# Performance work log

Hardware: AMD Instinct MI355X
Metric: run time of the kernel (lower is better)

The kernel has to match this reference:

```python
import jax, jax.numpy as jnp
import numpy as np

B, N, C0, L = 4, 16, 64, 2048
C1 = C2 = C3 = 128
E = 16384
EPS = 1e-5


def setup_inputs() -> dict:
    key = jax.random.key(0)
    ks = jax.random.split(key, 8)
    x = jax.random.normal(ks[0], (B, N, C0, L), jnp.float32)
    edge_index = jax.random.randint(ks[1], (2, E), 0, L, dtype=jnp.int64)

    def xavier(k, fi, fo):
        s = (2.0 / (fi + fo)) ** 0.5
        return jax.random.normal(k, (fi, fo), jnp.float32) * s

    return dict(
        x=x, edge_index=edge_index,
        W1=xavier(ks[2], C0, C1), b1=jnp.zeros(C1), g1=jnp.ones(C1), be1=jnp.zeros(C1),
        W2=xavier(ks[3], C1, C2), b2=jnp.zeros(C2), g2=jnp.ones(C2), be2=jnp.zeros(C2),
        W3=xavier(ks[4], C2, C3), b3=jnp.zeros(C3), g3=jnp.ones(C3), be3=jnp.zeros(C3),
    )


def _gcn(h, src, dst, norm, self_coef, W, bias):
    # h: [G, L, Cin] -> [G, L, Cout]; improved GCN: A_hat = A + 2I, sym-normalized
    hw = h @ W
    msgs = hw[:, src] * norm[None, :, None]          # [G, E, Cout]
    agg = jnp.zeros_like(hw).at[:, dst].add(msgs)     # scatter-add to targets
    return agg + self_coef[None, :, None] * hw + bias


def _center_bn_relu(h, g, be):
    # h: [G, L, C] -> [G, C, L]; mean-center over set dim n, BatchNorm1d (train), ReLU
    G, Lx, C = h.shape
    z = h.transpose(0, 2, 1).reshape(B, N, C, Lx)
    z = z - z.mean(axis=1, keepdims=True)
    z = z.reshape(G, C, Lx)
    mu = z.mean(axis=(0, 2), keepdims=True)
    var = z.var(axis=(0, 2), keepdims=True)           # biased, matches BN training
    z = (z - mu) / jnp.sqrt(var + EPS) * g[None, :, None] + be[None, :, None]
    return jnp.maximum(z, 0.0)


def reference(x, edge_index, W1, b1, g1, be1, W2, b2, g2, be2, W3, b3, g3, be3):
    b, n, c, l = x.shape
    src, dst = edge_index[0], edge_index[1]
    # improved=True: self-loop weight 2
    deg = jnp.zeros((l,), jnp.float32).at[dst].add(1.0) + 2.0
    dinv = 1.0 / jnp.sqrt(deg)
    norm = dinv[src] * dinv[dst]                      # per-edge coefficient
    self_coef = 2.0 * dinv * dinv                     # per-node self-loop coefficient

    h = x.reshape(b * n, c, l).transpose(0, 2, 1)     # [G, L, C0]

    h = _gcn(h, src, dst, norm, self_coef, W1, b1)
    z = _center_bn_relu(h, g1, be1)                   # [G, C1, L]
    h = z.transpose(0, 2, 1)

    h = _gcn(h, src, dst, norm, self_coef, W2, b2)
    z = _center_bn_relu(h, g2, be2)
    h = z.transpose(0, 2, 1)

    h = _gcn(h, src, dst, norm, self_coef, W3, b3)
    z = _center_bn_relu(h, g3, be3)                   # [G, C3, L]
    return z
```

## Files before the change

kernel.cpp:

```cpp
#include <hip/hip_runtime.h>
#include <hip/hip_bf16.h>

#define GG 64
#define LN 2048
#define BB 4
#define NS 16
#define EE 16384
#define C_0 64
#define CH 128
#define EPSV 1e-5f
#define VK 16
#define GNB 8
#define ECAP 384
#define SLICE ((size_t)LN * 1024)

using bf16x8 = __attribute__((ext_vector_type(8))) short;
using f32x4  = __attribute__((ext_vector_type(4))) float;
using u32x4  = __attribute__((ext_vector_type(4))) unsigned int;
typedef unsigned long long ull;

__device__ __forceinline__ float b2f(unsigned short u) {
    union { unsigned int i; float f; } v; v.i = ((unsigned int)u) << 16; return v.f;
}
__device__ __forceinline__ unsigned short f2b(float f) {
    union { float f; unsigned int i; } v; v.f = f;
    unsigned int r = v.i + 0x7fffu + ((v.i >> 16) & 1u);
    return (unsigned short)(r >> 16);
}
__device__ __forceinline__ void acc8(float* acc, u32x4 v, float w) {
    acc[0] += w * b2f((unsigned short)(v.x & 0xffffu));
    acc[1] += w * b2f((unsigned short)(v.x >> 16));
    acc[2] += w * b2f((unsigned short)(v.y & 0xffffu));
    acc[3] += w * b2f((unsigned short)(v.y >> 16));
    acc[4] += w * b2f((unsigned short)(v.z & 0xffffu));
    acc[5] += w * b2f((unsigned short)(v.z >> 16));
    acc[6] += w * b2f((unsigned short)(v.w & 0xffffu));
    acc[7] += w * b2f((unsigned short)(v.w >> 16));
}

__global__ void k_deg(const int* __restrict__ dst, int* __restrict__ cnt) {
    int e = blockIdx.x * blockDim.x + threadIdx.x;
    if (e < EE) atomicAdd(&cnt[dst[e]], 1);
}

__global__ void k_node(const int* __restrict__ cnt, float* __restrict__ dinv,
                       float* __restrict__ selfc) {
    int l = blockIdx.x * blockDim.x + threadIdx.x;
    if (l < LN) {
        float d = (float)cnt[l] + 2.0f;
        float di = rsqrtf(d);
        dinv[l] = di;
        selfc[l] = 2.0f * di * di;
    }
}

__global__ void k_scan(const int* __restrict__ cnt, int* __restrict__ off) {
    __shared__ int part[256];
    __shared__ int pre[256];
    int t = threadIdx.x;
    int base = t * 8;
    int loc[8];
    int s = 0;
#pragma unroll
    for (int i = 0; i < 8; i++) { loc[i] = cnt[base + i]; s += loc[i]; }
    part[t] = s;
    __syncthreads();
    if (t == 0) {
        int run = 0;
        for (int i = 0; i < 256; i++) { pre[i] = run; run += part[i]; }
        off[LN] = run;
    }
    __syncthreads();
    int run = pre[t];
#pragma unroll
    for (int i = 0; i < 8; i++) { off[base + i] = run; run += loc[i]; }
}

__global__ void k_fill(const int* __restrict__ src, const int* __restrict__ dst,
                       const int* __restrict__ off, int* __restrict__ cur,
                       const float* __restrict__ dinv, ull* __restrict__ epack) {
    int e = blockIdx.x * blockDim.x + threadIdx.x;
    if (e < EE) {
        int s = src[e], d = dst[e];
        int pos = atomicAdd(&cur[d], 1);
        int idx = off[d] + pos;
        union { float f; unsigned u; } w;
        w.f = dinv[s] * dinv[d];
        epack[idx] = (ull)(unsigned)s | ((ull)w.u << 32);
    }
}

__global__ void k_wprep(const float* __restrict__ W, unsigned short* __restrict__ Wp,
                        int K) {
    int idx = blockIdx.x * 256 + threadIdx.x;
    if (idx < K * CH) {
        int k = idx >> 7, c = idx & (CH - 1);
        int nf = c >> 4, lr = c & 15, ks = k >> 5, hi = (k >> 3) & 3, j = k & 7;
        Wp[(ks * 8 + nf) * 512 + (hi * 16 + lr) * 8 + j] = f2b(W[idx]);
    }
}

template <int K, bool FUSE>
__global__ __launch_bounds__(256) void k_mm(
    const float* __restrict__ X, const unsigned short* __restrict__ Ap,
    const float* __restrict__ scl, const float* __restrict__ bet,
    const unsigned short* __restrict__ Wp, unsigned short* __restrict__ hw)
{
    constexpr int KP = K + 8;
    __shared__ unsigned short As[64 * 136];
    const int g = blockIdx.y;
    const int l0 = blockIdx.x * 64;
    const int t = threadIdx.x;
    const int wq = t >> 6;
    const int lane = t & 63;
    const int lr = lane & 15;
    const int hi = lane >> 4;
    const int kof = hi * 8;

    f32x4 acc[8];
#pragma unroll
    for (int i = 0; i < 8; i++) acc[i] = (f32x4){0.f, 0.f, 0.f, 0.f};

    if (FUSE) {
        const int sg = g >> 5;
        const int gi = g & 31;
        const int row = l0 + wq * 16 + lr;
        bf16x8 aF[K / 32];
#pragma unroll
        for (int ks = 0; ks < K / 32; ks++) {
            const unsigned short* ap = Ap + (size_t)(sg * 4 + ks) * SLICE +
                                       (size_t)row * 1024 + gi * 32 + kof;
            union { uint4 v; unsigned short s[8]; } u;
            u.v = *(const uint4*)ap;
            const int cb = ks * 32 + kof;
            float4 s0 = *(const float4*)&scl[cb];
            float4 s1 = *(const float4*)&scl[cb + 4];
            float4 c0 = *(const float4*)&bet[cb];
            float4 c1 = *(const float4*)&bet[cb + 4];
            union { bf16x8 f; unsigned short s[8]; } o;
            o.s[0] = f2b(fmaxf(b2f(u.s[0]) * s0.x + c0.x, 0.f));
            o.s[1] = f2b(fmaxf(b2f(u.s[1]) * s0.y + c0.y, 0.f));
            o.s[2] = f2b(fmaxf(b2f(u.s[2]) * s0.z + c0.z, 0.f));
            o.s[3] = f2b(fmaxf(b2f(u.s[3]) * s0.w + c0.w, 0.f));
            o.s[4] = f2b(fmaxf(b2f(u.s[4]) * s1.x + c1.x, 0.f));
            o.s[5] = f2b(fmaxf(b2f(u.s[5]) * s1.y + c1.y, 0.f));
            o.s[6] = f2b(fmaxf(b2f(u.s[6]) * s1.z + c1.z, 0.f));
            o.s[7] = f2b(fmaxf(b2f(u.s[7]) * s1.w + c1.w, 0.f));
            aF[ks] = o.f;
        }
#pragma unroll
        for (int ks = 0; ks < K / 32; ks++) {
#pragma unroll
            for (int nf = 0; nf < 8; nf++) {
                bf16x8 bF = *(const bf16x8*)&Wp[(ks * 8 + nf) * 512 + lane * 8];
                acc[nf] = __builtin_amdgcn_mfma_f32_16x16x32_bf16(aF[ks], bF,
                                                                  acc[nf], 0, 0, 0);
            }
        }
    } else {
        const int k = t >> 2;
        const int lq = (t & 3) * 16;
        const float* xp = X + ((size_t)g * K + k) * LN + l0 + lq;
#pragma unroll
        for (int i = 0; i < 16; i += 4) {
            float4 v = *(const float4*)&xp[i];
            As[(lq + i + 0) * KP + k] = f2b(v.x);
            As[(lq + i + 1) * KP + k] = f2b(v.y);
            As[(lq + i + 2) * KP + k] = f2b(v.z);
            As[(lq + i + 3) * KP + k] = f2b(v.w);
        }
        __syncthreads();
#pragma unroll
        for (int ks = 0; ks < K / 32; ks++) {
            bf16x8 aF = *(const bf16x8*)&As[(wq * 16 + lr) * KP + ks * 32 + kof];
#pragma unroll
            for (int nf = 0; nf < 8; nf++) {
                bf16x8 bF = *(const bf16x8*)&Wp[(ks * 8 + nf) * 512 + lane * 8];
                acc[nf] = __builtin_amdgcn_mfma_f32_16x16x32_bf16(aF, bF,
                                                                  acc[nf], 0, 0, 0);
            }
        }
        __syncthreads();
    }
#pragma unroll
    for (int nf = 0; nf < 8; nf++) {
#pragma unroll
        for (int r = 0; r < 4; r++) {
            int row = wq * 16 + (lane >> 4) * 4 + r;
            int col = nf * 16 + lr;
            As[row * 136 + col] = f2b(acc[nf][r]);
        }
    }
    __syncthreads();
    {
        const int l = t >> 2;
        const int sc = t & 3;
        unsigned short* hp = hw + (size_t)((g >> 5) * 4 + sc) * SLICE +
                             (size_t)(l0 + l) * 1024 + (g & 31) * 32;
#pragma unroll
        for (int i = 0; i < 32; i += 8)
            *(uint4*)&hp[i] = *(const uint4*)&As[l * 136 + sc * 32 + i];
    }
}

__global__ __launch_bounds__(256) void k_gnv(
    const unsigned short* __restrict__ hw, unsigned short* __restrict__ a,
    float* __restrict__ varK, const int* __restrict__ off,
    const ull* __restrict__ epack, const float* __restrict__ selfc)
{
    __shared__ ull emeta[ECAP];
    __shared__ int soff[GNB + 1];
    __shared__ float sselfc[GNB];
    __shared__ float vred[4][32];
    const int bid = blockIdx.x;
    const int sid = bid & 7;
    const int chunk = bid >> 3;
    const int l0 = chunk * GNB;
    const int t = threadIdx.x;
    const int tr = t >> 7;
    const int ti = t & 127;
    const int lane = t & 63;
    const int wq = t >> 6;
    const int go = ti * 8;
    const unsigned short* hws = hw + sid * SLICE;
    unsigned short* aBs = a + sid * SLICE;

    u32x4 v0s[GNB / 2];
#pragma unroll
    for (int ii = 0; ii < GNB / 2; ii++)
        v0s[ii] = *(const u32x4*)&hws[(size_t)(l0 + ii * 2 + tr) * 1024 + go];

    const int e0 = off[l0];
    const int eTot = off[l0 + GNB] - e0;
    if (t <= GNB) soff[t] = off[l0 + t];
    if (t >= 32 && t < 32 + GNB) sselfc[t - 32] = selfc[l0 + t - 32];
    const int estg = eTot < ECAP ? eTot : ECAP;
    for (int i = t; i < estg; i += 256) emeta[i] = epack[e0 + i];
    __syncthreads();

    float vacc[8] = {0.f, 0.f, 0.f, 0.f, 0.f, 0.f, 0.f, 0.f};

    auto gather = [&](const ull* __restrict__ mp) {
#pragma unroll
        for (int ii = 0; ii < GNB / 2; ii++) {
            const int ln = ii * 2 + tr;
            const int l = l0 + ln;
            const int s0 = soff[ln] - e0;
            const int s1 = soff[ln + 1] - e0;
            const float sc = sselfc[ln];
            float acc[8];
            {
                u32x4 v0 = v0s[ii];
                acc[0] = sc * b2f((unsigned short)(v0.x & 0xffffu));
                acc[1] = sc * b2f((unsigned short)(v0.x >> 16));
                acc[2] = sc * b2f((unsigned short)(v0.y & 0xffffu));
                acc[3] = sc * b2f((unsigned short)(v0.y >> 16));
                acc[4] = sc * b2f((unsigned short)(v0.z & 0xffffu));
                acc[5] = sc * b2f((unsigned short)(v0.z >> 16));
                acc[6] = sc * b2f((unsigned short)(v0.w & 0xffffu));
                acc[7] = sc * b2f((unsigned short)(v0.w >> 16));
            }
            int e = s0;
            for (; e + 4 <= s1; e += 4) {
                ull m0 = mp[e], m1 = mp[e + 1], m2 = mp[e + 2], m3 = mp[e + 3];
                u32x4 vA = *(const u32x4*)&hws[(size_t)(unsigned)m0 * 1024 + go];
                u32x4 vB = *(const u32x4*)&hws[(size_t)(unsigned)m1 * 1024 + go];
                u32x4 vC = *(const u32x4*)&hws[(size_t)(unsigned)m2 * 1024 + go];
                u32x4 vD = *(const u32x4*)&hws[(size_t)(unsigned)m3 * 1024 + go];
                acc8(acc, vA, __uint_as_float((unsigned)(m0 >> 32)));
                acc8(acc, vB, __uint_as_float((unsigned)(m1 >> 32)));
                acc8(acc, vC, __uint_as_float((unsigned)(m2 >> 32)));
                acc8(acc, vD, __uint_as_float((unsigned)(m3 >> 32)));
            }
            for (; e < s1; e++) {
                ull m0 = mp[e];
                u32x4 vA = *(const u32x4*)&hws[(size_t)(unsigned)m0 * 1024 + go];
                acc8(acc, vA, __uint_as_float((unsigned)(m0 >> 32)));
            }
            float m[8];
#pragma unroll
            for (int j = 0; j < 8; j++) m[j] = acc[j];
#pragma unroll
            for (int mask = 4; mask <= 32; mask <<= 1) {
#pragma unroll
                for (int j = 0; j < 8; j++) m[j] += __shfl_xor(m[j], mask);
            }
            u32x4 o;
            unsigned short ob[8];
#pragma unroll
            for (int j = 0; j < 8; j++) {
                float d = acc[j] - m[j] * (1.f / NS);
                vacc[j] += d * d;
                ob[j] = f2b(d);
            }
            o.x = (unsigned int)ob[0] | ((unsigned int)ob[1] << 16);
            o.y = (unsigned int)ob[2] | ((unsigned int)ob[3] << 16);
            o.z = (unsigned int)ob[4] | ((unsigned int)ob[5] << 16);
            o.w = (unsigned int)ob[6] | ((unsigned int)ob[7] << 16);
            __builtin_nontemporal_store(o, (u32x4*)&aBs[(size_t)l * 1024 + go]);
        }
    };
    if (eTot <= ECAP) gather(emeta);
    else gather(epack + e0);

#pragma unroll
    for (int mask = 4; mask <= 32; mask <<= 1) {
#pragma unroll
        for (int j = 0; j < 8; j++) vacc[j] += __shfl_xor(vacc[j], mask);
    }
    if (lane < 4) {
#pragma unroll
        for (int j = 0; j < 8; j++) vred[wq][lane * 8 + j] = vacc[j];
    }
    __syncthreads();
    if (t < 32) {
        float s = vred[0][t] + vred[1][t] + vred[2][t] + vred[3][t];
        atomicAdd(&varK[(chunk & (VK - 1)) * CH + (sid & 3) * 32 + t], s);
    }
}

__global__ void k_scale(const float* __restrict__ varK, const float* __restrict__ gam,
                        float* __restrict__ scl) {
    int c = threadIdx.x;
    float v = 0.f;
#pragma unroll
    for (int k = 0; k < VK; k++) v += varK[k * CH + c];
    scl[c] = gam[c] * rsqrtf(v * (1.f / (GG * LN)) + EPSV);
}

__global__ __launch_bounds__(256) void k_epi_t(
    const unsigned short* __restrict__ a, const float* __restrict__ scl,
    const float* __restrict__ bet, float* __restrict__ out)
{
    __shared__ unsigned short lds[16 * 32 * 40];
    const int bid = blockIdx.x;
    const int sid = bid & 7;
    const int chunk = bid >> 3;
    const int l0 = chunk * 16;
    const int t = threadIdx.x;
    const int sg = sid >> 2;
    const int sc = sid & 3;
    const unsigned short* aBs = a + sid * SLICE;
    {
        const int tr = t >> 7;
        const int ti = t & 127;
        const int gl = ti >> 2;
        const int c0 = (ti & 3) * 8;
#pragma unroll
        for (int i = 0; i < 8; i++) {
            const int lloc = i * 2 + tr;
            uint4 v = *(const uint4*)&aBs[(size_t)(l0 + lloc) * 1024 + ti * 8];
            *(uint4*)&lds[(lloc * 32 + gl) * 40 + c0] = v;
        }
    }
    __syncthreads();
#pragma unroll
    for (int it = 0; it < 4; it++) {
        const int p = it * 256 + t;
        const int gl2 = p >> 5;
        const int c2 = p & 31;
        const int cG = sc * 32 + c2;
        const float s = scl[cG], bb = bet[cG];
        float o[16];
#pragma unroll
        for (int l = 0; l < 16; l++)
            o[l] = fmaxf(b2f(lds[(l * 32 + gl2) * 40 + c2]) * s + bb, 0.f);
        float* op = &out[((size_t)(sg * 32 + gl2) * CH + cG) * LN + l0];
#pragma unroll
        for (int l = 0; l < 16; l += 4)
            *(float4*)&op[l] = make_float4(o[l], o[l + 1], o[l + 2], o[l + 3]);
    }
}

extern "C" void kernel_launch(void* const* d_in, const int* in_sizes, int n_in,
                              void* d_out, int out_size, void* d_ws, size_t ws_size,
                              hipStream_t stream) {
    const float* x   = (const float*)d_in[0];
    const int*   ei  = (const int*)d_in[1];
    const float* W1  = (const float*)d_in[2];
    const float* g1  = (const float*)d_in[4];
    const float* be1 = (const float*)d_in[5];
    const float* W2  = (const float*)d_in[6];
    const float* g2  = (const float*)d_in[8];
    const float* be2 = (const float*)d_in[9];
    const float* W3  = (const float*)d_in[10];
    const float* g3  = (const float*)d_in[12];
    const float* be3 = (const float*)d_in[13];
    const int* srcp = ei;
    const int* dstp = ei + EE;

    char* ws = (char*)d_ws;
    size_t pos = 0;
    auto alloc = [&](size_t bytes) -> void* {
        void* p = ws + pos;
        pos = (pos + bytes + 255) & ~(size_t)255;
        return p;
    };
    const size_t big = (size_t)LN * GG * CH * sizeof(unsigned short);
    unsigned short* aB  = (unsigned short*)alloc(big);
    unsigned short* Wt1 = (unsigned short*)alloc(C_0 * CH * 2);
    unsigned short* Wt2 = (unsigned short*)alloc(CH * CH * 2);
    unsigned short* Wt3 = (unsigned short*)alloc(CH * CH * 2);
    int*   cnt   = (int*)alloc(LN * 4);
    int*   offA  = (int*)alloc((LN + 1) * 4);
    int*   cur   = (int*)alloc(LN * 4);
    float* dinv  = (float*)alloc(LN * 4);
    float* selfc = (float*)alloc(LN * 4);
    ull*   epack = (ull*)alloc(EE * 8);
    float* varK  = (float*)alloc(VK * CH * 4);
    float* scl   = (float*)alloc(CH * 4);
    unsigned short* hw = (ws_size >= pos + big) ? (unsigned short*)alloc(big)
                                                : (unsigned short*)d_out;

    hipMemsetAsync(cnt, 0, LN * 4, stream);
    hipMemsetAsync(cur, 0, LN * 4, stream);
    k_deg<<<EE / 256, 256, 0, stream>>>(dstp, cnt);
    k_node<<<LN / 256, 256, 0, stream>>>(cnt, dinv, selfc);
    k_scan<<<1, 256, 0, stream>>>(cnt, offA);
    k_fill<<<EE / 256, 256, 0, stream>>>(srcp, dstp, offA, cur, dinv, epack);
    k_wprep<<<(C_0 * CH) / 256, 256, 0, stream>>>(W1, Wt1, C_0);
    k_wprep<<<(CH * CH) / 256, 256, 0, stream>>>(W2, Wt2, CH);
    k_wprep<<<(CH * CH) / 256, 256, 0, stream>>>(W3, Wt3, CH);

    dim3 mmG(LN / 64, GG);
    const int gnvG = (LN / GNB) * 8;

    k_mm<C_0, false><<<mmG, 256, 0, stream>>>(x, nullptr, nullptr, nullptr, Wt1, hw);
    hipMemsetAsync(varK, 0, VK * CH * 4, stream);
    k_gnv<<<gnvG, 256, 0, stream>>>(hw, aB, varK, offA, epack, selfc);
    k_scale<<<1, CH, 0, stream>>>(varK, g1, scl);

    k_mm<CH, true><<<mmG, 256, 0, stream>>>(nullptr, aB, scl, be1, Wt2, hw);
    hipMemsetAsync(varK, 0, VK * CH * 4, stream);
    k_gnv<<<gnvG, 256, 0, stream>>>(hw, aB, varK, offA, epack, selfc);
    k_scale<<<1, CH, 0, stream>>>(varK, g2, scl);

    k_mm<CH, true><<<mmG, 256, 0, stream>>>(nullptr, aB, scl, be2, Wt3, hw);
    hipMemsetAsync(varK, 0, VK * CH * 4, stream);
    k_gnv<<<gnvG, 256, 0, stream>>>(hw, aB, varK, offA, epack, selfc);
    k_scale<<<1, CH, 0, stream>>>(varK, g3, scl);

    k_epi_t<<<128 * 8, 256, 0, stream>>>(aB, scl, be3, (float*)d_out);
}
```

Measured before the change: 244.2 us.

## Merge graph/weight prep into one kernel and fold BN scale into consumers

Replaces the degree, scan, fill and three weight-prep kernels plus two memsets with a single 7-block prep kernel. Graph CSR building now runs in one block using LDS atomics. The separate scale kernels and per-layer varK memsets are removed; each fused matmul and the epilogue recomputes the BN scale from the variance partials in LDS. The epilogue is also re-tiled to 32 rows by 16 groups per block. This cuts the launch count by about ten, at the cost of a serial single-block CSR build and redundant scale computation in every block.

```diff
diff --git a/kernel.cpp b/kernel.cpp
--- a/kernel.cpp
+++ b/kernel.cpp
@@ -37,77 +37,95 @@
     acc[6] += w * b2f((unsigned short)(v.w & 0xffffu));
     acc[7] += w * b2f((unsigned short)(v.w >> 16));
 }
-
-__global__ void k_deg(const int* __restrict__ dst, int* __restrict__ cnt) {
-    int e = blockIdx.x * blockDim.x + threadIdx.x;
-    if (e < EE) atomicAdd(&cnt[dst[e]], 1);
-}
-
-__global__ void k_node(const int* __restrict__ cnt, float* __restrict__ dinv,
-                       float* __restrict__ selfc) {
-    int l = blockIdx.x * blockDim.x + threadIdx.x;
-    if (l < LN) {
-        float d = (float)cnt[l] + 2.0f;
-        float di = rsqrtf(d);
-        dinv[l] = di;
-        selfc[l] = 2.0f * di * di;
-    }
-}
-
-__global__ void k_scan(const int* __restrict__ cnt, int* __restrict__ off) {
-    __shared__ int part[256];
-    __shared__ int pre[256];
-    int t = threadIdx.x;
-    int base = t * 8;
-    int loc[8];
-    int s = 0;
-#pragma unroll
-    for (int i = 0; i < 8; i++) { loc[i] = cnt[base + i]; s += loc[i]; }
-    part[t] = s;
-    __syncthreads();
-    if (t == 0) {
-        int run = 0;
-        for (int i = 0; i < 256; i++) { pre[i] = run; run += part[i]; }
-        off[LN] = run;
-    }
-    __syncthreads();
-    int run = pre[t];
-#pragma unroll
-    for (int i = 0; i < 8; i++) { off[base + i] = run; run += loc[i]; }
-}
-
-__global__ void k_fill(const int* __restrict__ src, const int* __restrict__ dst,
-                       const int* __restrict__ off, int* __restrict__ cur,
-                       const float* __restrict__ dinv, ull* __restrict__ epack) {
-    int e = blockIdx.x * blockDim.x + threadIdx.x;
-    if (e < EE) {
-        int s = src[e], d = dst[e];
-        int pos = atomicAdd(&cur[d], 1);
-        int idx = off[d] + pos;
-        union { float f; unsigned u; } w;
-        w.f = dinv[s] * dinv[d];
-        epack[idx] = (ull)(unsigned)s | ((ull)w.u << 32);
-    }
-}
-
-__global__ void k_wprep(const float* __restrict__ W, unsigned short* __restrict__ Wp,
-                        int K) {
-    int idx = blockIdx.x * 256 + threadIdx.x;
-    if (idx < K * CH) {
-        int k = idx >> 7, c = idx & (CH - 1);
-        int nf = c >> 4, lr = c & 15, ks = k >> 5, hi = (k >> 3) & 3, j = k & 7;
-        Wp[(ks * 8 + nf) * 512 + (hi * 16 + lr) * 8 + j] = f2b(W[idx]);
+__device__ __forceinline__ void wprep_one(const float* __restrict__ W,
+                                          unsigned short* __restrict__ Wp, int idx) {
+    int k = idx >> 7, c = idx & (CH - 1);
+    int nf = c >> 4, lr = c & 15, ks = k >> 5, hi = (k >> 3) & 3, j = k & 7;
+    Wp[(ks * 8 + nf) * 512 + (hi * 16 + lr) * 8 + j] = f2b(W[idx]);
+}
+
+__global__ __launch_bounds__(256) void k_prep(
+    const int* __restrict__ src, const int* __restrict__ dst,
+    const float* __restrict__ W1, const float* __restrict__ W2,
+    const float* __restrict__ W3,
+    float* __restrict__ selfc, int* __restrict__ off, ull* __restrict__ epack,
+    unsigned short* __restrict__ Wp1, unsigned short* __restrict__ Wp2,
+    unsigned short* __restrict__ Wp3, float* __restrict__ varK3)
+{
+    const int bid = blockIdx.x;
+    const int t = threadIdx.x;
+    if (bid == 0) {
+        __shared__ int cntL[LN];
+        __shared__ float dinvL[LN];
+        __shared__ int offL[LN + 1];
+        __shared__ int part[256];
+        __shared__ int pre2[256];
+        for (int i = t; i < LN; i += 256) cntL[i] = 0;
+        __syncthreads();
+        for (int e = t; e < EE; e += 256) atomicAdd(&cntL[dst[e]], 1);
+        __syncthreads();
+        for (int i = t; i < LN; i += 256) {
+            float d = (float)cntL[i] + 2.0f;
+            float di = rsqrtf(d);
+            dinvL[i] = di;
+            selfc[i] = 2.0f * di * di;
+        }
+        {
+            const int base = t * 8;
+            int loc[8];
+            int s = 0;
+#pragma unroll
+            for (int i = 0; i < 8; i++) { loc[i] = cntL[base + i]; s += loc[i]; }
+            part[t] = s;
+            __syncthreads();
+            if (t == 0) {
+                int run = 0;
+                for (int i = 0; i < 256; i++) { pre2[i] = run; run += part[i]; }
+                offL[LN] = run;
+                off[LN] = run;
+            }
+            __syncthreads();
+            int run = pre2[t];
+#pragma unroll
+            for (int i = 0; i < 8; i++) {
+                offL[base + i] = run;
+                off[base + i] = run;
+                run += loc[i];
+            }
+        }
+        __syncthreads();
+        for (int i = t; i < LN; i += 256) cntL[i] = 0;
+        __syncthreads();
+        for (int e = t; e < EE; e += 256) {
+            int s = src[e], d = dst[e];
+            int pos = atomicAdd(&cntL[d], 1);
+            union { float f; unsigned u; } w;
+            w.f = dinvL[s] * dinvL[d];
+            epack[offL[d] + pos] = (ull)(unsigned)s | ((ull)w.u << 32);
+        }
+    } else if (bid == 1) {
+        for (int i = t; i < C_0 * CH; i += 256) wprep_one(W1, Wp1, i);
+    } else if (bid <= 3) {
+        const int base = (bid - 2) * 8192;
+        for (int i = t; i < 8192; i += 256) wprep_one(W2, Wp2, base + i);
+    } else if (bid <= 5) {
+        const int base = (bid - 4) * 8192;
+        for (int i = t; i < 8192; i += 256) wprep_one(W3, Wp3, base + i);
+    } else {
+        for (int i = t; i < 3 * VK * CH; i += 256) varK3[i] = 0.f;
     }
 }
 
 template <int K, bool FUSE>
 __global__ __launch_bounds__(256) void k_mm(
     const float* __restrict__ X, const unsigned short* __restrict__ Ap,
-    const float* __restrict__ scl, const float* __restrict__ bet,
+    const float* __restrict__ varKp, const float* __restrict__ gam,
+    const float* __restrict__ bet,
     const unsigned short* __restrict__ Wp, unsigned short* __restrict__ hw)
 {
     constexpr int KP = K + 8;
     __shared__ unsigned short As[64 * 136];
+    __shared__ float sclL[CH];
     const int g = blockIdx.y;
     const int l0 = blockIdx.x * 64;
     const int t = threadIdx.x;
@@ -122,6 +140,13 @@
     for (int i = 0; i < 8; i++) acc[i] = (f32x4){0.f, 0.f, 0.f, 0.f};
 
     if (FUSE) {
+        if (t < CH) {
+            float v = 0.f;
+#pragma unroll
+            for (int k = 0; k < VK; k++) v += varKp[k * CH + t];
+            sclL[t] = gam[t] * rsqrtf(v * (1.f / (GG * LN)) + EPSV);
+        }
+        __syncthreads();
         const int sg = g >> 5;
         const int gi = g & 31;
         const int row = l0 + wq * 16 + lr;
@@ -133,8 +158,8 @@
             union { uint4 v; unsigned short s[8]; } u;
             u.v = *(const uint4*)ap;
             const int cb = ks * 32 + kof;
-            float4 s0 = *(const float4*)&scl[cb];
-            float4 s1 = *(const float4*)&scl[cb + 4];
+            float4 s0 = *(const float4*)&sclL[cb];
+            float4 s1 = *(const float4*)&sclL[cb + 4];
             float4 c0 = *(const float4*)&bet[cb];
             float4 c1 = *(const float4*)&bet[cb + 4];
             union { bf16x8 f; unsigned short s[8]; } o;
@@ -319,55 +344,57 @@
     }
 }
 
-__global__ void k_scale(const float* __restrict__ varK, const float* __restrict__ gam,
-                        float* __restrict__ scl) {
-    int c = threadIdx.x;
-    float v = 0.f;
-#pragma unroll
-    for (int k = 0; k < VK; k++) v += varK[k * CH + c];
-    scl[c] = gam[c] * rsqrtf(v * (1.f / (GG * LN)) + EPSV);
-}
-
 __global__ __launch_bounds__(256) void k_epi_t(
-    const unsigned short* __restrict__ a, const float* __restrict__ scl,
-    const float* __restrict__ bet, float* __restrict__ out)
+    const unsigned short* __restrict__ a, const float* __restrict__ varKp,
+    const float* __restrict__ gam, const float* __restrict__ bet,
+    float* __restrict__ out)
 {
-    __shared__ unsigned short lds[16 * 32 * 40];
+    __shared__ unsigned short lds[32 * 16 * 40];
+    __shared__ float sclL[CH];
     const int bid = blockIdx.x;
     const int sid = bid & 7;
-    const int chunk = bid >> 3;
-    const int l0 = chunk * 16;
+    const int q = bid >> 3;
+    const int gh = q & 1;
+    const int chunk = q >> 1;
+    const int l0 = chunk * 32;
     const int t = threadIdx.x;
     const int sg = sid >> 2;
     const int sc = sid & 3;
     const unsigned short* aBs = a + sid * SLICE;
+    if (t < CH) {
+        float v = 0.f;
+#pragma unroll
+        for (int k = 0; k < VK; k++) v += varKp[k * CH + t];
+        sclL[t] = gam[t] * rsqrtf(v * (1.f / (GG * LN)) + EPSV);
+    }
     {
-        const int tr = t >> 7;
-        const int ti = t & 127;
+        const int qr = t >> 6;
+        const int ti = t & 63;
         const int gl = ti >> 2;
         const int c0 = (ti & 3) * 8;
 #pragma unroll
         for (int i = 0; i < 8; i++) {
-            const int lloc = i * 2 + tr;
-            uint4 v = *(const uint4*)&aBs[(size_t)(l0 + lloc) * 1024 + ti * 8];
-            *(uint4*)&lds[(lloc * 32 + gl) * 40 + c0] = v;
+            const int lrow = i * 4 + qr;
+            uint4 v = *(const uint4*)&aBs[(size_t)(l0 + lrow) * 1024 + gh * 512 + ti * 8];
+            *(uint4*)&lds[(lrow * 16 + gl) * 40 + c0] = v;
         }
     }
     __syncthreads();
 #pragma unroll
-    for (int it = 0; it < 4; it++) {
+    for (int it = 0; it < 2; it++) {
         const int p = it * 256 + t;
-        const int gl2 = p >> 5;
+        const int g2 = p >> 5;
         const int c2 = p & 31;
         const int cG = sc * 32 + c2;
-        const float s = scl[cG], bb = bet[cG];
-        float o[16];
-#pragma unroll
-        for (int l = 0; l < 16; l++)
-            o[l] = fmaxf(b2f(lds[(l * 32 + gl2) * 40 + c2]) * s + bb, 0.f);
-        float* op = &out[((size_t)(sg * 32 + gl2) * CH + cG) * LN + l0];
-#pragma unroll
-        for (int l = 0; l < 16; l += 4)
+        const int gG = sg * 32 + gh * 16 + g2;
+        const float s = sclL[cG], bb = bet[cG];
+        float o[32];
+#pragma unroll
+        for (int l = 0; l < 32; l++)
+            o[l] = fmaxf(b2f(lds[(l * 16 + g2) * 40 + c2]) * s + bb, 0.f);
+        float* op = &out[((size_t)gG * CH + cG) * LN + l0];
+#pragma unroll
+        for (int l = 0; l < 32; l += 4)
             *(float4*)&op[l] = make_float4(o[l], o[l + 1], o[l + 2], o[l + 3]);
     }
 }
@@ -398,47 +425,34 @@
     };
     const size_t big = (size_t)LN * GG * CH * sizeof(unsigned short);
     unsigned short* aB  = (unsigned short*)alloc(big);
-    unsigned short* Wt1 = (unsigned short*)alloc(C_0 * CH * 2);
-    unsigned short* Wt2 = (unsigned short*)alloc(CH * CH * 2);
-    unsigned short* Wt3 = (unsigned short*)alloc(CH * CH * 2);
-    int*   cnt   = (int*)alloc(LN * 4);
+    unsigned short* Wp1 = (unsigned short*)alloc(C_0 * CH * 2);
+    unsigned short* Wp2 = (unsigned short*)alloc(CH * CH * 2);
+    unsigned short* Wp3 = (unsigned short*)alloc(CH * CH * 2);
     int*   offA  = (int*)alloc((LN + 1) * 4);
-    int*   cur   = (int*)alloc(LN * 4);
-    float* dinv  = (float*)alloc(LN * 4);
     float* selfc = (float*)alloc(LN * 4);
     ull*   epack = (ull*)alloc(EE * 8);
-    float* varK  = (float*)alloc(VK * CH * 4);
-    float* scl   = (float*)alloc(CH * 4);
+    float* varK3 = (float*)alloc(3 * VK * CH * 4);
     unsigned short* hw = (ws_size >= pos + big) ? (unsigned short*)alloc(big)
                                                 : (unsigned short*)d_out;
 
-    hipMemsetAsync(cnt, 0, LN * 4, stream);
-    hipMemsetAsync(cur, 0, LN * 4, stream);
-    k_deg<<<EE / 256, 256, 0, stream>>>(dstp, cnt);
-    k_node<<<LN / 256, 256, 0, stream>>>(cnt, dinv, selfc);
-    k_scan<<<1, 256, 0, stream>>>(cnt, offA);
-    k_fill<<<EE / 256, 256, 0, stream>>>(srcp, dstp, offA, cur, dinv, epack);
-    k_wprep<<<(C_0 * CH) / 256, 256, 0, stream>>>(W1, Wt1, C_0);
-    k_wprep<<<(CH * CH) / 256, 256, 0, stream>>>(W2, Wt2, CH);
-    k_wprep<<<(CH * CH) / 256, 256, 0, stream>>>(W3, Wt3, CH);
+    k_prep<<<7, 256, 0, stream>>>(srcp, dstp, W1, W2, W3, selfc, offA, epack,
+                                  Wp1, Wp2, Wp3, varK3);
 
     dim3 mmG(LN / 64, GG);
     const int gnvG = (LN / GNB) * 8;
-
-    k_mm<C_0, false><<<mmG, 256, 0, stream>>>(x, nullptr, nullptr, nullptr, Wt1, hw);
-    hipMemsetAsync(varK, 0, VK * CH * 4, stream);
-    k_gnv<<<gnvG, 256, 0, stream>>>(hw, aB, varK, offA, epack, selfc);
-    k_scale<<<1, CH, 0, stream>>>(varK, g1, scl);
-
-    k_mm<CH, true><<<mmG, 256, 0, stream>>>(nullptr, aB, scl, be1, Wt2, hw);
-    hipMemsetAsync(varK, 0, VK * CH * 4, stream);
-    k_gnv<<<gnvG, 256, 0, stream>>>(hw, aB, varK, offA, epack, selfc);
-    k_scale<<<1, CH, 0, stream>>>(varK, g2, scl);
-
-    k_mm<CH, true><<<mmG, 256, 0, stream>>>(nullptr, aB, scl, be2, Wt3, hw);
-    hipMemsetAsync(varK, 0, VK * CH * 4, stream);
-    k_gnv<<<gnvG, 256, 0, stream>>>(hw, aB, varK, offA, epack, selfc);
-    k_scale<<<1, CH, 0, stream>>>(varK, g3, scl);
-
-    k_epi_t<<<128 * 8, 256, 0, stream>>>(aB, scl, be3, (float*)d_out);
-}
+    float* vK1 = varK3;
+    float* vK2 = varK3 + VK * CH;
+    float* vK3 = varK3 + 2 * VK * CH;
+
+    k_mm<C_0, false><<<mmG, 256, 0, stream>>>(x, nullptr, nullptr, nullptr, nullptr,
+                                              Wp1, hw);
+    k_gnv<<<gnvG, 256, 0, stream>>>(hw, aB, vK1, offA, epack, selfc);
+
+    k_mm<CH, true><<<mmG, 256, 0, stream>>>(nullptr, aB, vK1, g1, be1, Wp2, hw);
+    k_gnv<<<gnvG, 256, 0, stream>>>(hw, aB, vK2, offA, epack, selfc);
+
+    k_mm<CH, true><<<mmG, 256, 0, stream>>>(nullptr, aB, vK2, g2, be2, Wp3, hw);
+    k_gnv<<<gnvG, 256, 0, stream>>>(hw, aB, vK3, offA, epack, selfc);
+
+    k_epi_t<<<64 * 2 * 8, 256, 0, stream>>>(aB, vK3, g3, be3, (float*)d_out);
+}
```

Result: slower. 255.8 us (+4.7%).
